# Performance work log

Measured on AMD Instinct MI355X. Metric: run time of the kernel, lower is better.

Reference implementation:

```python
import jax, jax.numpy as jnp
import numpy as np

N = 100000
E = 1600000
IN_DIM = 256
HID = 128


def setup_inputs() -> dict:
    key = jax.random.key(0)
    k = jax.random.split(key, 8)
    x = jax.random.normal(k[0], (N, IN_DIM), dtype=jnp.float32)
    edge_index = jax.random.randint(k[1], (2, E), 0, N, dtype=jnp.int64 if jax.config.jax_enable_x64 else jnp.int32)
    # GCNConv weight (no bias pre-aggregation; bias added after aggregation, as in PyG)
    W_conv = jax.random.normal(k[2], (IN_DIM, HID), dtype=jnp.float32) / np.sqrt(IN_DIM)
    b_conv = jnp.zeros((HID,), dtype=jnp.float32)
    prelu_a = jnp.full((1,), 0.25, dtype=jnp.float32)  # torch.nn.PReLU default init
    W_lin = jax.random.normal(k[3], (HID, IN_DIM), dtype=jnp.float32) / np.sqrt(HID)
    b_lin = jnp.zeros((IN_DIM,), dtype=jnp.float32)
    return {"x": x, "edge_index": edge_index, "W_conv": W_conv, "b_conv": b_conv,
            "prelu_a": prelu_a, "W_lin": W_lin, "b_lin": b_lin}


def _gcn_conv(x, edge_index, W, b):
    # h = x @ W  ([N, HID])
    h = x @ W
    src, dst = edge_index[0], edge_index[1]
    # add self-loops
    loops = jnp.arange(N, dtype=src.dtype)
    src = jnp.concatenate([src, loops])
    dst = jnp.concatenate([dst, loops])
    # symmetric degree normalization deg^-1/2 (degree over incoming edges incl. self-loops)
    deg = jax.ops.segment_sum(jnp.ones_like(dst, dtype=h.dtype), dst, num_segments=N)
    dinv = jnp.where(deg > 0, jax.lax.rsqrt(deg), 0.0)
    norm = dinv[src] * dinv[dst]                     # [E+N]
    msg = h[src] * norm[:, None]                     # gather + scale  [E+N, HID]
    out = jax.ops.segment_sum(msg, dst, num_segments=N)  # scatter-add  [N, HID]
    return out + b


def reference(x, edge_index, W_conv, b_conv, prelu_a, W_lin, b_lin):
    h = _gcn_conv(x, edge_index, W_conv, b_conv)
    h = jnp.where(h >= 0, h, prelu_a * h)            # PReLU (single shared slope)
    # dropout p=0.0 -> identity
    return h @ W_lin + b_lin                          # [N, IN_DIM]
```

## Files before the change

### kernel.cpp

```cpp
#include <hip/hip_runtime.h>

#define N_NODES 100000
#define E_EDGES 1600000
#define INDIM 256
#define HID 128
#define CAP 64
#define NPART 8
#define PART_SZ 12500
#define ECAP 32768
#define PA_BLOCKS 1563
#define PA_STRIDE (PA_BLOCKS * 256)
#define G1_BLOCKS 1563
#define PB_BLOCKS 1024

typedef __attribute__((ext_vector_type(8))) short s16x8;
typedef __attribute__((ext_vector_type(4))) float f32x4;

__device__ __forceinline__ unsigned short cvt_bf16(float f) {
    unsigned int u = __float_as_uint(f);
    u += 0x7FFFu + ((u >> 16) & 1u);
    return (unsigned short)(u >> 16);
}
__device__ __forceinline__ float bf16_to_f(unsigned short s) {
    return __uint_as_float(((unsigned int)s) << 16);
}

__global__ __launch_bounds__(256) void parta_kernel(const int* __restrict__ src,
                                                    const int* __restrict__ dst,
                                                    int* __restrict__ gcnt,
                                                    unsigned int* __restrict__ pedges,
                                                    const float* __restrict__ Wc,
                                                    const float* __restrict__ Wl,
                                                    unsigned short* __restrict__ f1,
                                                    unsigned short* __restrict__ f2) {
    __shared__ int sCount[8];
    __shared__ int sBase[8];
    const int tid = threadIdx.x;

    if (blockIdx.x < 256) {
        int pt = blockIdx.x * 256 + tid;
        if (pt < 32768) {
            int j = pt & 7, L = (pt >> 3) & 63, t = (pt >> 9) & 7, c = pt >> 12;
            int k = c * 32 + ((L >> 4) * 8) + j;
            int n = t * 16 + (L & 15);
            f1[pt] = cvt_bf16(Wc[k * 128 + n]);
        } else {
            int u = pt - 32768;
            int j = u & 7, L = (u >> 3) & 63, t = (u >> 9) & 15, c = u >> 13;
            int k = c * 32 + ((L >> 4) * 8) + j;
            int n = t * 16 + (L & 15);
            f2[u] = cvt_bf16(Wl[k * 256 + n]);
        }
    }

    if (tid < 8) sCount[tid] = 0;
    __syncthreads();
    const int lane = tid & 63;
    const int t0 = blockIdx.x * 256 + tid;
    const int xcd = blockIdx.x & 7;

    unsigned int pk[4];
    int pp[4];
    int lo[4];
#pragma unroll
    for (int r = 0; r < 4; ++r) {
        int e = t0 + r * PA_STRIDE;
        bool valid = e < E_EDGES;
        int d = 0, s = 0;
        if (valid) { d = dst[e]; s = src[e]; }
        int p = valid ? d / PART_SZ : 8;
        unsigned long long mask_p = 0ull;
#pragma unroll
        for (int v = 0; v < 8; ++v) {
            unsigned long long mv = __ballot(p == v);
            if (p == v) mask_p = mv;
        }
        int off = __popcll(mask_p & ((1ull << lane) - 1ull));
        int ldr = (mask_p == 0ull) ? 0 : (__ffsll(mask_p) - 1);
        int wbase = 0;
        if (valid && lane == ldr) wbase = atomicAdd(&sCount[p], __popcll(mask_p));
        wbase = __shfl(wbase, ldr);
        pp[r] = p;
        lo[r] = wbase + off;
        pk[r] = ((unsigned int)(d - p * PART_SZ) << 17) | (unsigned int)s;
    }
    __syncthreads();
    if (tid < 8) sBase[tid] = atomicAdd(&gcnt[xcd * 8 + tid], sCount[tid]);
    __syncthreads();
#pragma unroll
    for (int r = 0; r < 4; ++r) {
        if (pp[r] < 8) {
            int pos = sBase[pp[r]] + lo[r];
            if (pos < ECAP)
                pedges[(size_t)(xcd * 8 + pp[r]) * ECAP + pos] = pk[r];
        }
    }
}

__global__ __launch_bounds__(256) void fat_kernel(const float* __restrict__ x,
                                                  const unsigned short* __restrict__ fragW,
                                                  unsigned short* __restrict__ h,
                                                  const unsigned int* __restrict__ pedges,
                                                  const int* __restrict__ gcnt,
                                                  int* __restrict__ count,
                                                  int* __restrict__ bucket) {
    __shared__ __align__(16) unsigned short xs[64 * 48];
    const int tid = threadIdx.x;

    if (blockIdx.x < G1_BLOCKS) {
        const int r0 = blockIdx.x * 64;
        const int w = tid >> 6, lane = tid & 63;
        const int q = lane >> 4, m = lane & 15;
        const int srow = tid >> 2, skg = tid & 3;

        f32x4 acc[8];
#pragma unroll
        for (int t = 0; t < 8; ++t) acc[t] = (f32x4){0.f, 0.f, 0.f, 0.f};

        const s16x8* fwv = (const s16x8*)fragW;

        for (int c = 0; c < 8; ++c) {
            int gr = r0 + srow;
            float4 v0 = make_float4(0.f, 0.f, 0.f, 0.f), v1 = v0;
            if (gr < N_NODES) {
                const float* p = &x[(size_t)gr * INDIM + c * 32 + skg * 8];
                v0 = *(const float4*)p;
                v1 = *(const float4*)(p + 4);
            }
            uint4 pk;
            pk.x = ((unsigned)cvt_bf16(v0.y) << 16) | cvt_bf16(v0.x);
            pk.y = ((unsigned)cvt_bf16(v0.w) << 16) | cvt_bf16(v0.z);
            pk.z = ((unsigned)cvt_bf16(v1.y) << 16) | cvt_bf16(v1.x);
            pk.w = ((unsigned)cvt_bf16(v1.w) << 16) | cvt_bf16(v1.z);
            *(uint4*)&xs[srow * 48 + skg * 8] = pk;
            __syncthreads();

            s16x8 a = *(const s16x8*)&xs[(w * 16 + m) * 48 + q * 8];
#pragma unroll
            for (int t = 0; t < 8; ++t) {
                s16x8 b = fwv[(c * 8 + t) * 64 + lane];
                acc[t] = __builtin_amdgcn_mfma_f32_16x16x32_bf16(a, b, acc[t], 0, 0, 0);
            }
            __syncthreads();
        }

        const int row_base = r0 + w * 16 + q * 4;
#pragma unroll
        for (int t = 0; t < 8; ++t) {
#pragma unroll
            for (int r = 0; r < 4; ++r) {
                int row = row_base + r;
                if (row < N_NODES) h[(size_t)row * HID + t * 16 + m] = cvt_bf16(acc[t][r]);
            }
        }
    } else {
        const int part = blockIdx.x & 7;
        const int bslot = (blockIdx.x - G1_BLOCKS) >> 3;
#pragma unroll
        for (int xx = 0; xx < 8; ++xx) {
            int n = gcnt[xx * 8 + part];
            if (n > ECAP) n = ECAP;
            const unsigned int* lst = pedges + (size_t)(xx * 8 + part) * ECAP;
            for (int i = bslot * 256 + tid; i < n; i += (PB_BLOCKS / 8) * 256) {
                unsigned int v = lst[i];
                int s = (int)(v & 0x1FFFFu);
                int d = part * PART_SZ + (int)(v >> 17);
                int slot = atomicAdd(&count[d], 1);
                if (slot < CAP) bucket[d * CAP + slot] = s;
            }
        }
    }
}

__global__ __launch_bounds__(256) void gather_kernel(const int* __restrict__ bucket,
                                                     const int* __restrict__ count,
                                                     const unsigned short* __restrict__ h,
                                                     const float* __restrict__ b_conv,
                                                     const float* __restrict__ prelu_a,
                                                     unsigned short* __restrict__ agg) {
    const int part = blockIdx.x & 7;
    const int bidx = blockIdx.x >> 3;
    const int wv = threadIdx.x >> 6;
    const int wid = part * PART_SZ + bidx * 4 + wv;
    const int lane = threadIdx.x & 63;
    const int g = lane >> 4;
    const int l = lane & 15;
    const int raw = count[wid];
    const float dn = rsqrtf((float)(raw + 1));
    int deg = raw > CAP ? CAP : raw;
    const uint4* hp4 = (const uint4*)h;

    int s_l = wid;
    float dv_l = 0.f;
    if (lane < deg) {
        s_l = bucket[wid * CAP + lane];
        dv_l = rsqrtf((float)(count[s_l] + 1));
    }

    float acc[8];
    {
        uint4 hv = hp4[(size_t)wid * 16 + l];
        float w0 = (g == 0) ? dn * dn : 0.f;
        const unsigned int* pv = (const unsigned int*)&hv;
#pragma unroll
        for (int k = 0; k < 4; ++k) {
            acc[2 * k]     = w0 * bf16_to_f((unsigned short)(pv[k] & 0xFFFF));
            acc[2 * k + 1] = w0 * bf16_to_f((unsigned short)(pv[k] >> 16));
        }
    }

    for (int j = 0; j < deg; j += 8) {
        int e0 = j + g;
        int e1 = j + 4 + g;
        int s0 = __shfl(s_l, e0);
        int s1 = __shfl(s_l, e1);
        float w0 = __shfl(dv_l, e0) * dn;
        float w1 = __shfl(dv_l, e1) * dn;
        uint4 hv0 = hp4[(size_t)s0 * 16 + l];
        uint4 hv1 = hp4[(size_t)s1 * 16 + l];
        const unsigned int* p0 = (const unsigned int*)&hv0;
        const unsigned int* p1 = (const unsigned int*)&hv1;
#pragma unroll
        for (int k = 0; k < 4; ++k) {
            acc[2 * k]     += w0 * bf16_to_f((unsigned short)(p0[k] & 0xFFFF));
            acc[2 * k + 1] += w0 * bf16_to_f((unsigned short)(p0[k] >> 16));
        }
#pragma unroll
        for (int k = 0; k < 4; ++k) {
            acc[2 * k]     += w1 * bf16_to_f((unsigned short)(p1[k] & 0xFFFF));
            acc[2 * k + 1] += w1 * bf16_to_f((unsigned short)(p1[k] >> 16));
        }
    }

#pragma unroll
    for (int k = 0; k < 8; ++k) {
        acc[k] += __shfl_xor(acc[k], 16);
        acc[k] += __shfl_xor(acc[k], 32);
    }

    if (g == 0) {
        float a = prelu_a[0];
        float4 b0 = *(const float4*)&b_conv[l * 8];
        float4 b1 = *(const float4*)&b_conv[l * 8 + 4];
        float bc[8] = {b0.x, b0.y, b0.z, b0.w, b1.x, b1.y, b1.z, b1.w};
        unsigned int o[4];
#pragma unroll
        for (int k = 0; k < 4; ++k) {
            float ox = acc[2 * k] + bc[2 * k];
            float oy = acc[2 * k + 1] + bc[2 * k + 1];
            ox = ox >= 0.f ? ox : a * ox;
            oy = oy >= 0.f ? oy : a * oy;
            o[k] = ((unsigned)cvt_bf16(oy) << 16) | cvt_bf16(ox);
        }
        uint4 ov;
        ov.x = o[0]; ov.y = o[1]; ov.z = o[2]; ov.w = o[3];
        ((uint4*)agg)[(size_t)wid * 16 + l] = ov;
    }
}

__global__ __launch_bounds__(256) void gemm2_kernel(const unsigned short* __restrict__ agg,
                                                    const unsigned short* __restrict__ fragW,
                                                    const float* __restrict__ b_lin,
                                                    float* __restrict__ out) {
    __shared__ __align__(16) unsigned short xs[64 * 48];
    const int tid = threadIdx.x;
    const int r0 = blockIdx.x * 64;
    const int w = tid >> 6, lane = tid & 63;
    const int q = lane >> 4, m = lane & 15;
    const int srow = tid >> 2, skg = tid & 3;

    f32x4 acc[16];
#pragma unroll
    for (int t = 0; t < 16; ++t) acc[t] = (f32x4){0.f, 0.f, 0.f, 0.f};

    const s16x8* fwv = (const s16x8*)fragW;
    const uint4* aggv = (const uint4*)agg;

    for (int c = 0; c < 4; ++c) {
        int gr = r0 + srow;
        uint4 pk = make_uint4(0u, 0u, 0u, 0u);
        if (gr < N_NODES) pk = aggv[(size_t)gr * 16 + c * 4 + skg];
        *(uint4*)&xs[srow * 48 + skg * 8] = pk;
        __syncthreads();

        s16x8 a = *(const s16x8*)&xs[(w * 16 + m) * 48 + q * 8];
#pragma unroll
        for (int t = 0; t < 16; ++t) {
            s16x8 b = fwv[(c * 16 + t) * 64 + lane];
            acc[t] = __builtin_amdgcn_mfma_f32_16x16x32_bf16(a, b, acc[t], 0, 0, 0);
        }
        __syncthreads();
    }

    const int row_base = r0 + w * 16 + q * 4;
#pragma unroll
    for (int t = 0; t < 16; ++t) {
        float bias = b_lin[t * 16 + m];
#pragma unroll
        for (int r = 0; r < 4; ++r) {
            int row = row_base + r;
            if (row < N_NODES) out[(size_t)row * INDIM + t * 16 + m] = acc[t][r] + bias;
        }
    }
}

extern "C" void kernel_launch(void* const* d_in, const int* in_sizes, int n_in,
                              void* d_out, int out_size, void* d_ws, size_t ws_size,
                              hipStream_t stream) {
    const float* x       = (const float*)d_in[0];
    const int*   eidx    = (const int*)d_in[1];
    const float* W_conv  = (const float*)d_in[2];
    const float* b_conv  = (const float*)d_in[3];
    const float* prelu_a = (const float*)d_in[4];
    const float* W_lin   = (const float*)d_in[5];
    const float* b_lin   = (const float*)d_in[6];
    float* out = (float*)d_out;

    const int* src = eidx;
    const int* dst = eidx + E_EDGES;

    char* base = (char*)d_ws;
    int*   bucket = (int*)base;
    unsigned short* agg = (unsigned short*)(base + (size_t)N_NODES * CAP * 4);
    int*   count  = (int*)((char*)agg + (size_t)N_NODES * HID * 2);
    int*   gcnt   = count + 100000;
    unsigned short* fragW1 = (unsigned short*)(count + 100352);
    unsigned short* fragW2 = fragW1 + 32768;
    unsigned int* pedges = (unsigned int*)agg;

    unsigned short* h = (unsigned short*)d_out;

    hipMemsetAsync(count, 0, (size_t)100352 * sizeof(int), stream);

    parta_kernel<<<PA_BLOCKS, 256, 0, stream>>>(src, dst, gcnt, pedges,
                                                W_conv, W_lin, fragW1, fragW2);

    fat_kernel<<<G1_BLOCKS + PB_BLOCKS, 256, 0, stream>>>(x, fragW1, h,
                                                          pedges, gcnt, count, bucket);

    gather_kernel<<<NPART * (PART_SZ / 4), 256, 0, stream>>>(
        bucket, count, h, b_conv, prelu_a, agg);

    gemm2_kernel<<<(N_NODES + 63) / 64, 256, 0, stream>>>(agg, fragW2, b_lin, out);
}
```

Measured before the change: 389.1 us.

## Regroup kernel stages and use nontemporal loads/stores for streaming data

Replaces the memset with a small prep kernel that also converts the weights to bf16 fragments. Edge partitioning now runs inside the same launch as the first GEMM, and the bucket-fill pass moves to its own kernel. Streaming global accesses (edges, x, h, agg, out) switch to nontemporal builtins. The intent is to overlap edge partitioning with GEMM1 and to cut cache pollution. The cost is an extra kernel launch, and nontemporal hints may hurt where data is reused, such as h being read in gather.

After: 412.0 us. +5.9%, slower.

```diff
diff --git a/kernel.cpp b/kernel.cpp
--- a/kernel.cpp
+++ b/kernel.cpp
@@ -15,6 +15,7 @@
 
 typedef __attribute__((ext_vector_type(8))) short s16x8;
 typedef __attribute__((ext_vector_type(4))) float f32x4;
+typedef __attribute__((ext_vector_type(4))) unsigned int u32x4;
 
 __device__ __forceinline__ unsigned short cvt_bf16(float f) {
     unsigned int u = __float_as_uint(f);
@@ -25,20 +26,15 @@
     return __uint_as_float(((unsigned int)s) << 16);
 }
 
-__global__ __launch_bounds__(256) void parta_kernel(const int* __restrict__ src,
-                                                    const int* __restrict__ dst,
-                                                    int* __restrict__ gcnt,
-                                                    unsigned int* __restrict__ pedges,
-                                                    const float* __restrict__ Wc,
-                                                    const float* __restrict__ Wl,
-                                                    unsigned short* __restrict__ f1,
-                                                    unsigned short* __restrict__ f2) {
-    __shared__ int sCount[8];
-    __shared__ int sBase[8];
+__global__ __launch_bounds__(256) void prepzero_kernel(const float* __restrict__ Wc,
+                                                       const float* __restrict__ Wl,
+                                                       unsigned short* __restrict__ f1,
+                                                       unsigned short* __restrict__ f2,
+                                                       int* __restrict__ count) {
+    const int b = blockIdx.x;
     const int tid = threadIdx.x;
-
-    if (blockIdx.x < 256) {
-        int pt = blockIdx.x * 256 + tid;
+    if (b < 256) {
+        int pt = b * 256 + tid;
         if (pt < 32768) {
             int j = pt & 7, L = (pt >> 3) & 63, t = (pt >> 9) & 7, c = pt >> 12;
             int k = c * 32 + ((L >> 4) * 8) + j;
@@ -51,64 +47,72 @@
             int n = t * 16 + (L & 15);
             f2[u] = cvt_bf16(Wl[k * 256 + n]);
         }
-    }
-
-    if (tid < 8) sCount[tid] = 0;
-    __syncthreads();
-    const int lane = tid & 63;
-    const int t0 = blockIdx.x * 256 + tid;
-    const int xcd = blockIdx.x & 7;
-
-    unsigned int pk[4];
-    int pp[4];
-    int lo[4];
-#pragma unroll
-    for (int r = 0; r < 4; ++r) {
-        int e = t0 + r * PA_STRIDE;
-        bool valid = e < E_EDGES;
-        int d = 0, s = 0;
-        if (valid) { d = dst[e]; s = src[e]; }
-        int p = valid ? d / PART_SZ : 8;
-        unsigned long long mask_p = 0ull;
-#pragma unroll
-        for (int v = 0; v < 8; ++v) {
-            unsigned long long mv = __ballot(p == v);
-            if (p == v) mask_p = mv;
-        }
-        int off = __popcll(mask_p & ((1ull << lane) - 1ull));
-        int ldr = (mask_p == 0ull) ? 0 : (__ffsll(mask_p) - 1);
-        int wbase = 0;
-        if (valid && lane == ldr) wbase = atomicAdd(&sCount[p], __popcll(mask_p));
-        wbase = __shfl(wbase, ldr);
-        pp[r] = p;
-        lo[r] = wbase + off;
-        pk[r] = ((unsigned int)(d - p * PART_SZ) << 17) | (unsigned int)s;
-    }
-    __syncthreads();
-    if (tid < 8) sBase[tid] = atomicAdd(&gcnt[xcd * 8 + tid], sCount[tid]);
-    __syncthreads();
-#pragma unroll
-    for (int r = 0; r < 4; ++r) {
-        if (pp[r] < 8) {
-            int pos = sBase[pp[r]] + lo[r];
-            if (pos < ECAP)
-                pedges[(size_t)(xcd * 8 + pp[r]) * ECAP + pos] = pk[r];
-        }
-    }
-}
-
-__global__ __launch_bounds__(256) void fat_kernel(const float* __restrict__ x,
-                                                  const unsigned short* __restrict__ fragW,
-                                                  unsigned short* __restrict__ h,
-                                                  const unsigned int* __restrict__ pedges,
-                                                  const int* __restrict__ gcnt,
-                                                  int* __restrict__ count,
-                                                  int* __restrict__ bucket) {
+    } else {
+        for (int i = (b - 256) * 256 + tid; i < 100352; i += 256 * 256) count[i] = 0;
+    }
+}
+
+__global__ __launch_bounds__(256) void fata_kernel(const int* __restrict__ src,
+                                                   const int* __restrict__ dst,
+                                                   int* __restrict__ gcnt,
+                                                   unsigned int* __restrict__ pedges,
+                                                   const float* __restrict__ x,
+                                                   const unsigned short* __restrict__ fragW,
+                                                   unsigned short* __restrict__ h) {
     __shared__ __align__(16) unsigned short xs[64 * 48];
+    __shared__ int sCount[8];
+    __shared__ int sBase[8];
     const int tid = threadIdx.x;
 
-    if (blockIdx.x < G1_BLOCKS) {
-        const int r0 = blockIdx.x * 64;
+    if (blockIdx.x < PA_BLOCKS) {
+        if (tid < 8) sCount[tid] = 0;
+        __syncthreads();
+        const int lane = tid & 63;
+        const int t0 = blockIdx.x * 256 + tid;
+        const int xcd = blockIdx.x & 7;
+
+        unsigned int pk[4];
+        int pp[4];
+        int lo[4];
+#pragma unroll
+        for (int r = 0; r < 4; ++r) {
+            int e = t0 + r * PA_STRIDE;
+            bool valid = e < E_EDGES;
+            int d = 0, s = 0;
+            if (valid) {
+                d = __builtin_nontemporal_load(dst + e);
+                s = __builtin_nontemporal_load(src + e);
+            }
+            int p = valid ? d / PART_SZ : 8;
+            unsigned long long mask_p = 0ull;
+#pragma unroll
+            for (int v = 0; v < 8; ++v) {
+                unsigned long long mv = __ballot(p == v);
+                if (p == v) mask_p = mv;
+            }
+            int off = __popcll(mask_p & ((1ull << lane) - 1ull));
+            int ldr = (mask_p == 0ull) ? 0 : (__ffsll(mask_p) - 1);
+            int wbase = 0;
+            if (valid && lane == ldr) wbase = atomicAdd(&sCount[p], __popcll(mask_p));
+            wbase = __shfl(wbase, ldr);
+            pp[r] = p;
+            lo[r] = wbase + off;
+            pk[r] = ((unsigned int)(d - p * PART_SZ) << 17) | (unsigned int)s;
+        }
+        __syncthreads();
+        if (tid < 8) sBase[tid] = atomicAdd(&gcnt[xcd * 8 + tid], sCount[tid]);
+        __syncthreads();
+#pragma unroll
+        for (int r = 0; r < 4; ++r) {
+            if (pp[r] < 8) {
+                int pos = sBase[pp[r]] + lo[r];
+                if (pos < ECAP)
+                    __builtin_nontemporal_store(pk[r],
+                        pedges + (size_t)(xcd * 8 + pp[r]) * ECAP + pos);
+            }
+        }
+    } else {
+        const int r0 = (blockIdx.x - PA_BLOCKS) * 64;
         const int w = tid >> 6, lane = tid & 63;
         const int q = lane >> 4, m = lane & 15;
         const int srow = tid >> 2, skg = tid & 3;
@@ -121,11 +125,11 @@
 
         for (int c = 0; c < 8; ++c) {
             int gr = r0 + srow;
-            float4 v0 = make_float4(0.f, 0.f, 0.f, 0.f), v1 = v0;
+            f32x4 v0 = (f32x4){0.f, 0.f, 0.f, 0.f}, v1 = v0;
             if (gr < N_NODES) {
-                const float* p = &x[(size_t)gr * INDIM + c * 32 + skg * 8];
-                v0 = *(const float4*)p;
-                v1 = *(const float4*)(p + 4);
+                const f32x4* p = (const f32x4*)&x[(size_t)gr * INDIM + c * 32 + skg * 8];
+                v0 = __builtin_nontemporal_load(p);
+                v1 = __builtin_nontemporal_load(p + 1);
             }
             uint4 pk;
             pk.x = ((unsigned)cvt_bf16(v0.y) << 16) | cvt_bf16(v0.x);
@@ -150,24 +154,32 @@
 #pragma unroll
             for (int r = 0; r < 4; ++r) {
                 int row = row_base + r;
-                if (row < N_NODES) h[(size_t)row * HID + t * 16 + m] = cvt_bf16(acc[t][r]);
-            }
-        }
-    } else {
-        const int part = blockIdx.x & 7;
-        const int bslot = (blockIdx.x - G1_BLOCKS) >> 3;
-#pragma unroll
-        for (int xx = 0; xx < 8; ++xx) {
-            int n = gcnt[xx * 8 + part];
-            if (n > ECAP) n = ECAP;
-            const unsigned int* lst = pedges + (size_t)(xx * 8 + part) * ECAP;
-            for (int i = bslot * 256 + tid; i < n; i += (PB_BLOCKS / 8) * 256) {
-                unsigned int v = lst[i];
-                int s = (int)(v & 0x1FFFFu);
-                int d = part * PART_SZ + (int)(v >> 17);
-                int slot = atomicAdd(&count[d], 1);
-                if (slot < CAP) bucket[d * CAP + slot] = s;
-            }
+                if (row < N_NODES)
+                    __builtin_nontemporal_store(cvt_bf16(acc[t][r]),
+                        h + (size_t)row * HID + t * 16 + m);
+            }
+        }
+    }
+}
+
+__global__ __launch_bounds__(256) void partb_kernel(const unsigned int* __restrict__ pedges,
+                                                    const int* __restrict__ gcnt,
+                                                    int* __restrict__ count,
+                                                    int* __restrict__ bucket) {
+    const int part = blockIdx.x & 7;
+    const int bslot = blockIdx.x >> 3;
+    const int tid = threadIdx.x;
+#pragma unroll
+    for (int xx = 0; xx < 8; ++xx) {
+        int n = gcnt[xx * 8 + part];
+        if (n > ECAP) n = ECAP;
+        const unsigned int* lst = pedges + (size_t)(xx * 8 + part) * ECAP;
+        for (int i = bslot * 256 + tid; i < n; i += (PB_BLOCKS / 8) * 256) {
+            unsigned int v = __builtin_nontemporal_load(lst + i);
+            int s = (int)(v & 0x1FFFFu);
+            int d = part * PART_SZ + (int)(v >> 17);
+            int slot = atomicAdd(&count[d], 1);
+            if (slot < CAP) bucket[d * CAP + slot] = s;
         }
     }
 }
@@ -274,13 +286,13 @@
     for (int t = 0; t < 16; ++t) acc[t] = (f32x4){0.f, 0.f, 0.f, 0.f};
 
     const s16x8* fwv = (const s16x8*)fragW;
-    const uint4* aggv = (const uint4*)agg;
+    const u32x4* aggv = (const u32x4*)agg;
 
     for (int c = 0; c < 4; ++c) {
         int gr = r0 + srow;
-        uint4 pk = make_uint4(0u, 0u, 0u, 0u);
-        if (gr < N_NODES) pk = aggv[(size_t)gr * 16 + c * 4 + skg];
-        *(uint4*)&xs[srow * 48 + skg * 8] = pk;
+        u32x4 pk = (u32x4){0u, 0u, 0u, 0u};
+        if (gr < N_NODES) pk = __builtin_nontemporal_load(&aggv[(size_t)gr * 16 + c * 4 + skg]);
+        *(u32x4*)&xs[srow * 48 + skg * 8] = pk;
         __syncthreads();
 
         s16x8 a = *(const s16x8*)&xs[(w * 16 + m) * 48 + q * 8];
@@ -299,7 +311,9 @@
 #pragma unroll
         for (int r = 0; r < 4; ++r) {
             int row = row_base + r;
-            if (row < N_NODES) out[(size_t)row * INDIM + t * 16 + m] = acc[t][r] + bias;
+            if (row < N_NODES)
+                __builtin_nontemporal_store(acc[t][r] + bias,
+                    out + (size_t)row * INDIM + t * 16 + m);
         }
     }
 }
@@ -330,13 +344,12 @@
 
     unsigned short* h = (unsigned short*)d_out;
 
-    hipMemsetAsync(count, 0, (size_t)100352 * sizeof(int), stream);
-
-    parta_kernel<<<PA_BLOCKS, 256, 0, stream>>>(src, dst, gcnt, pedges,
-                                                W_conv, W_lin, fragW1, fragW2);
-
-    fat_kernel<<<G1_BLOCKS + PB_BLOCKS, 256, 0, stream>>>(x, fragW1, h,
-                                                          pedges, gcnt, count, bucket);
+    prepzero_kernel<<<512, 256, 0, stream>>>(W_conv, W_lin, fragW1, fragW2, count);
+
+    fata_kernel<<<PA_BLOCKS + G1_BLOCKS, 256, 0, stream>>>(src, dst, gcnt, pedges,
+                                                           x, fragW1, h);
+
+    partb_kernel<<<PB_BLOCKS, 256, 0, stream>>>(pedges, gcnt, count, bucket);
 
     gather_kernel<<<NPART * (PART_SZ / 4), 256, 0, stream>>>(
         bucket, count, h, b_conv, prelu_a, agg);
```
